# Performance work log

Measured on AMD Instinct MI355X. Metric: run time of the kernel, lower is better.

## Reference

```python
import jax, jax.numpy as jnp
import numpy as np

T = 2048          # num tokens (single long prefill sequence)
HID = 2048        # hidden_size
NH = 16           # num query heads
NKV = 2           # num kv heads
HD = 128          # head_dim (kv_channels)
ROPE_BASE = 10000.0


def setup_inputs() -> dict:
    key = jax.random.key(0)
    k1, k2, k3, k4, k5 = jax.random.split(key, 5)
    s = 0.02
    return {
        "hidden_states": jax.random.normal(k1, (T, HID), dtype=jnp.float32),
        "positions": jnp.arange(T, dtype=jnp.int64 if jax.config.jax_enable_x64 else jnp.int32),
        "Wq": jax.random.normal(k2, (NH * HD, HID), dtype=jnp.float32) * s,
        "Wk": jax.random.normal(k3, (NKV * HD, HID), dtype=jnp.float32) * s,
        "Wv": jax.random.normal(k4, (NKV * HD, HID), dtype=jnp.float32) * s,
        "Wo": jax.random.normal(k5, (HID, NH * HD), dtype=jnp.float32) * s,
    }


def _rope_cos_sin(positions):
    # fp32 RoPE tables, HF-style (concat of freqs with itself)
    inv_freq = 1.0 / (ROPE_BASE ** (jnp.arange(0, HD, 2, dtype=jnp.float32) / HD))
    freqs = positions.astype(jnp.float32)[:, None] * inv_freq[None, :]   # [T, HD/2]
    emb = jnp.concatenate([freqs, freqs], axis=-1)                        # [T, HD]
    return jnp.cos(emb)[:, None, :], jnp.sin(emb)[:, None, :]             # [T,1,HD]


def _rotate_half(x):
    x1, x2 = jnp.split(x, 2, axis=-1)
    return jnp.concatenate([-x2, x1], axis=-1)


def reference(hidden_states, positions, Wq, Wk, Wv, Wo):
    dtype = hidden_states.dtype
    # fused QKV projection (weights concatenated once, single GEMM)
    W_fused = jnp.concatenate([Wq, Wk, Wv], axis=0)            # [q+2kv, HID]
    qkv = hidden_states @ W_fused.T                             # [T, q+2kv]
    q, k, v = jnp.split(qkv, [NH * HD, NH * HD + NKV * HD], axis=-1)

    # fp32 RoPE on q/k
    cos, sin = _rope_cos_sin(positions)                         # [T,1,HD]
    qf = q.reshape(T, NH, HD).astype(jnp.float32)
    kf = k.reshape(T, NKV, HD).astype(jnp.float32)
    qf = qf * cos + _rotate_half(qf) * sin
    kf = kf * cos + _rotate_half(kf) * sin
    q = qf.astype(dtype)                                        # [T,NH,HD]
    k = kf.astype(dtype)                                        # [T,NKV,HD]
    v = v.reshape(T, NKV, HD)

    # causal GQA attention (same math as the paged-attention kernel on one seq)
    group = NH // NKV
    k_rep = jnp.repeat(k, group, axis=1)                        # [T,NH,HD]
    v_rep = jnp.repeat(v, group, axis=1)                        # [T,NH,HD]
    scale = HD ** -0.5
    scores = jnp.einsum('qhd,khd->hqk', q, k_rep) * scale       # [NH,T,T]
    causal = jnp.tril(jnp.ones((T, T), dtype=bool))
    scores = jnp.where(causal[None], scores, jnp.finfo(scores.dtype).min)
    probs = jax.nn.softmax(scores, axis=-1)
    attn = jnp.einsum('hqk,khd->qhd', probs, v_rep).reshape(T, NH * HD)

    return attn @ Wo.T                                          # [T, HID]
```

## Files before the change

### kernel.cpp

```cpp
#include <hip/hip_runtime.h>

#define T_TOK 2048
#define HID   2048
#define NH    16
#define NKV   2
#define HD    128
#define QDIM  (NH * HD)
#define KVDIM (NKV * HD)
#define QKVDIM (QDIM + 2 * KVDIM)

typedef float          f32x4  __attribute__((ext_vector_type(4)));
typedef unsigned short u16x8  __attribute__((ext_vector_type(8)));
typedef __bf16         bf16x8 __attribute__((ext_vector_type(8)));

__device__ __forceinline__ unsigned short f2bf(float f) {
    __bf16 h = (__bf16)f;
    return __builtin_bit_cast(unsigned short, h);
}
__device__ __forceinline__ float bf2f(unsigned short u) {
    return (float)__builtin_bit_cast(__bf16, u);
}

__device__ __forceinline__ f32x4 mfma16(u16x8 a, u16x8 b, f32x4 c) {
    return __builtin_amdgcn_mfma_f32_16x16x32_bf16(
        __builtin_bit_cast(bf16x8, a), __builtin_bit_cast(bf16x8, b), c, 0, 0, 0);
}

#define QSCL 0.12751743f
#define DEFER_THR 11.5416f

__global__ __launch_bounds__(256) void pack_bf16_all(
    const float* __restrict__ hidden, const float* __restrict__ Wq,
    const float* __restrict__ Wk, const float* __restrict__ Wv,
    const float* __restrict__ Wo,
    unsigned short* __restrict__ hb, unsigned short* __restrict__ Wf,
    unsigned short* __restrict__ Wob)
{
    const int b = blockIdx.x;
    const float* src; unsigned short* dst; size_t off;
    if      (b < 2048) { src = hidden; dst = hb;            off = (size_t)b * 2048; }
    else if (b < 4096) { src = Wq;     dst = Wf;            off = (size_t)(b - 2048) * 2048; }
    else if (b < 4352) { src = Wk;     dst = Wf + 4194304;  off = (size_t)(b - 4096) * 2048; }
    else if (b < 4608) { src = Wv;     dst = Wf + 4718592;  off = (size_t)(b - 4352) * 2048; }
    else               { src = Wo;     dst = Wob;           off = (size_t)(b - 4608) * 2048; }

    const size_t i = off + threadIdx.x * 8;
    float4 f0 = *reinterpret_cast<const float4*>(src + i);
    float4 f1 = *reinterpret_cast<const float4*>(src + i + 4);
    u16x8 o;
    o[0]=f2bf(f0.x); o[1]=f2bf(f0.y); o[2]=f2bf(f0.z); o[3]=f2bf(f0.w);
    o[4]=f2bf(f1.x); o[5]=f2bf(f1.y); o[6]=f2bf(f1.z); o[7]=f2bf(f1.w);
    *reinterpret_cast<u16x8*>(dst + i) = o;
}

template<bool BF16OUT>
__global__ __launch_bounds__(256) void gemm_bf16(
    const unsigned short* __restrict__ A,
    const unsigned short* __restrict__ B,
    void* __restrict__ Cv,
    int K, int NC, int nbx)
{
    __shared__ alignas(16) unsigned short As[2][128 * 64];
    __shared__ alignas(16) unsigned short Bs[2][128 * 64];

    const int tid  = threadIdx.x;
    const int lane = tid & 63;
    const int w    = tid >> 6;
    const int lg   = lane >> 4, lc = lane & 15;

    const int cpx = gridDim.x >> 3;
    const int wg  = (blockIdx.x & 7) * cpx + (blockIdx.x >> 3);
    const int m0  = (wg / nbx) * 128, n0 = (wg % nbx) * 128;

    const int rowL = lane >> 3;
    const int gS   = (lane & 7) ^ rowL;
    const int wr   = (w >> 1) * 64, wc = (w & 1) * 64;

    f32x4 acc[4][4] = {};

    auto stage = [&](int buf, int kb) {
        #pragma unroll
        for (int ci = 0; ci < 4; ci++) {
            const int chunk = w * 4 + ci;
            const int row   = chunk * 8 + rowL;
            const unsigned short* gpA = &A[(size_t)(m0 + row) * K + kb + gS * 8];
            __builtin_amdgcn_global_load_lds(
                (const __attribute__((address_space(1))) void*)gpA,
                (__attribute__((address_space(3))) void*)(&As[buf][chunk * 512]),
                16, 0, 0);
            const unsigned short* gpB = &B[(size_t)(n0 + row) * K + kb + gS * 8];
            __builtin_amdgcn_global_load_lds(
                (const __attribute__((address_space(1))) void*)gpB,
                (__attribute__((address_space(3))) void*)(&Bs[buf][chunk * 512]),
                16, 0, 0);
        }
    };

    stage(0, 0);
    const int nk = K >> 6;
    for (int t = 0; t < nk; ++t) {
        if (t + 1 < nk) {
            stage((t + 1) & 1, (t + 1) * 64);
            asm volatile("s_waitcnt vmcnt(8)" ::: "memory");
        } else {
            asm volatile("s_waitcnt vmcnt(0)" ::: "memory");
        }
        __syncthreads();

        const unsigned short* As_ = As[t & 1];
        const unsigned short* Bs_ = Bs[t & 1];
        #pragma unroll
        for (int kk = 0; kk < 2; kk++) {
            u16x8 af[4], bf[4];
            #pragma unroll
            for (int mi = 0; mi < 4; mi++) {
                const int r = wr + mi * 16 + lc;
                const int g = (kk * 4 + lg) ^ (lc & 7);
                af[mi] = *reinterpret_cast<const u16x8*>(&As_[r * 64 + g * 8]);
            }
            #pragma unroll
            for (int ni = 0; ni < 4; ni++) {
                const int r = wc + ni * 16 + lc;
                const int g = (kk * 4 + lg) ^ (lc & 7);
                bf[ni] = *reinterpret_cast<const u16x8*>(&Bs_[r * 64 + g * 8]);
            }
            #pragma unroll
            for (int mi = 0; mi < 4; mi++)
                #pragma unroll
                for (int ni = 0; ni < 4; ni++)
                    acc[mi][ni] = mfma16(af[mi], bf[ni], acc[mi][ni]);
        }
        __syncthreads();
    }

    #pragma unroll
    for (int mi = 0; mi < 4; mi++)
        #pragma unroll
        for (int ni = 0; ni < 4; ni++)
            #pragma unroll
            for (int j = 0; j < 4; j++) {
                const size_t idx = (size_t)(m0 + wr + mi * 16 + lg * 4 + j) * NC
                                   + n0 + wc + ni * 16 + lc;
                if constexpr (BF16OUT)
                    ((unsigned short*)Cv)[idx] = f2bf(acc[mi][ni][j]);
                else
                    ((float*)Cv)[idx] = acc[mi][ni][j];
            }
}

__global__ __launch_bounds__(256) void rope_kernel(
    const unsigned short* __restrict__ qkvb,
    const int* __restrict__ positions,
    unsigned short* __restrict__ qr,
    unsigned short* __restrict__ kr)
{
    const int t   = blockIdx.x;
    const int tid = threadIdx.x;
    __shared__ float cosv[64], sinv[64];

    if (tid < 64) {
        float invf = expf(-(float)tid * 0.14391156831212787f);
        float f = (float)positions[t] * invf;
        cosv[tid] = cosf(f);
        sinv[tid] = sinf(f);
    }
    __syncthreads();

    const unsigned short* row = qkvb + (size_t)t * QKVDIM;

    for (int i = tid; i < NH * 64; i += 256) {
        int hh = i >> 6, j = i & 63;
        float x1 = bf2f(row[hh * HD + j]);
        float x2 = bf2f(row[hh * HD + j + 64]);
        float c = cosv[j], s = sinv[j];
        qr[(size_t)t * QDIM + hh * HD + j]      = f2bf((x1 * c - x2 * s) * QSCL);
        qr[(size_t)t * QDIM + hh * HD + j + 64] = f2bf((x2 * c + x1 * s) * QSCL);
    }
    if (tid < NKV * 64) {
        int hh = tid >> 6, j = tid & 63;
        float x1 = bf2f(row[QDIM + hh * HD + j]);
        float x2 = bf2f(row[QDIM + hh * HD + j + 64]);
        float c = cosv[j], s = sinv[j];
        kr[(size_t)t * KVDIM + hh * HD + j]      = f2bf(x1 * c - x2 * s);
        kr[(size_t)t * KVDIM + hh * HD + j + 64] = f2bf(x2 * c + x1 * s);
    }
}

__global__ __launch_bounds__(256) void v_transpose(
    const unsigned short* __restrict__ qkvb,
    unsigned short* __restrict__ vt)
{
    __shared__ unsigned short tile[64][72];
    const int tid = threadIdx.x;
    const int t0  = blockIdx.x * 64;
    const int d0  = blockIdx.y * 64;

    {
        int r = tid >> 2;
        int c = (tid & 3) * 16;
        const unsigned short* src =
            &qkvb[(size_t)(t0 + r) * QKVDIM + QDIM + KVDIM + d0 + c];
        *reinterpret_cast<u16x8*>(&tile[r][c])     = *reinterpret_cast<const u16x8*>(src);
        *reinterpret_cast<u16x8*>(&tile[r][c + 8]) = *reinterpret_cast<const u16x8*>(src + 8);
    }
    __syncthreads();
    {
        int dr = tid >> 3;
        int tc = (tid & 7) * 8;
        #pragma unroll
        for (int i = 0; i < 2; i++) {
            int d = dr + i * 32;
            u16x8 ov;
            #pragma unroll
            for (int e = 0; e < 8; e++) ov[e] = tile[tc + e][d];
            *reinterpret_cast<u16x8*>(&vt[(size_t)(d0 + d) * T_TOK + t0 + tc]) = ov;
        }
    }
}

__global__ __launch_bounds__(256) void attn_kernel(
    const unsigned short* __restrict__ q,
    const unsigned short* __restrict__ k,
    const unsigned short* __restrict__ vt,
    unsigned short* __restrict__ o,
    float* __restrict__ pO,
    float* __restrict__ pML)
{
    __shared__ alignas(16) unsigned short Ks[2][64 * 128];
    __shared__ alignas(16) unsigned short Vs[2][128 * 64];
    __shared__ alignas(16) unsigned short P[4][16][72];

    const int tid  = threadIdx.x;
    const int lane = tid & 63;
    const int w    = tid >> 6;
    const int lg   = lane >> 4, lc = lane & 15;
    const int b    = blockIdx.x;
    const int h    = b & 15;
    const int idx  = b >> 4;

    int tau, c0;
    if (idx <= 16)      { tau = 15 + idx; c0 = 0; }
    else if (idx == 17) { tau = 31;       c0 = 1; }
    else {
        int j = idx - 18, kk = 15 - (j >> 1);
        if ((j & 1) == 0) { tau = kk - 1;  c0 = 0; }
        else              { tau = kk + 15; c0 = 1; }
    }
    const int kstart = c0 << 4;
    const int kcnt   = min(16, tau + 1 - kstart);

    const int q0   = tau * 64 + w * 16;
    const int hk   = h >> 3;
    const int xr   = (lc & 7) << 4;

    const int krow_l = (lane >> 4);
    const int kgS    = (lane & 15);
    const int vrow_l = (lane >> 3);
    const int vgS    = (lane & 7);

    u16x8 qf[4];
    #pragma unroll
    for (int dc = 0; dc < 4; dc++)
        qf[dc] = *reinterpret_cast<const u16x8*>(
            &q[(size_t)(q0 + lc) * QDIM + h * HD + dc * 32 + lg * 8]);

    float mrow = -1e30f, ell = 0.f;
    f32x4 oacc[8] = {};

    auto stage = [&](int buf, int kb) {
        #pragma unroll
        for (int ci = 0; ci < 4; ci++) {
            const int chunk = w * 4 + ci;
            const int row   = chunk * 4 + krow_l;
            const int gSk   = kgS ^ (row & 7);
            const unsigned short* gp =
                &k[(size_t)(kb + row) * KVDIM + hk * HD + gSk * 8];
            __builtin_amdgcn_global_load_lds(
                (const __attribute__((address_space(1))) void*)gp,
                (__attribute__((address_space(3))) void*)(&Ks[buf][chunk * 512]),
                16, 0, 0);
        }
        #pragma unroll
        for (int ci = 0; ci < 4; ci++) {
            const int chunk = w * 4 + ci;
            const int dr    = chunk * 8 + vrow_l;
            const int gSv   = vgS ^ (dr & 7);
            const unsigned short* gp =
                &vt[(size_t)(hk * HD + dr) * T_TOK + kb + gSv * 8];
            __builtin_amdgcn_global_load_lds(
                (const __attribute__((address_space(1))) void*)gp,
                (__attribute__((address_space(3))) void*)(&Vs[buf][chunk * 512]),
                16, 0, 0);
        }
    };

    stage(0, kstart * 64);
    for (int it = 0; it < kcnt; ++it) {
        if (it + 1 < kcnt) {
            stage((it + 1) & 1, (kstart + it + 1) * 64);
            asm volatile("s_waitcnt vmcnt(8)" ::: "memory");
        } else {
            asm volatile("s_waitcnt vmcnt(0)" ::: "memory");
        }
        __syncthreads();

        const int kb = (kstart + it) * 64;
        const char* KsB = (const char*)Ks[it & 1];
        const char* VsB = (const char*)Vs[it & 1];

        float sc[4][4];
        const bool dia = (kb + 63 > q0);
        #pragma unroll
        for (int c4 = 0; c4 < 4; c4++) {
            const int row = c4 * 16 + lc;
            f32x4 s = {0.f, 0.f, 0.f, 0.f};
            #pragma unroll
            for (int dc = 0; dc < 4; dc++) {
                u16x8 kf = *reinterpret_cast<const u16x8*>(
                    KsB + row * 256 + ((dc * 64 + lg * 16) ^ xr));
                s = mfma16(kf, qf[dc], s);
            }
            if (dia) {
                #pragma unroll
                for (int j = 0; j < 4; j++) {
                    const int kpos = kb + c4 * 16 + lg * 4 + j;
                    sc[c4][j] = (kpos <= q0 + lc) ? s[j] : -1e30f;
                }
            } else {
                #pragma unroll
                for (int j = 0; j < 4; j++) sc[c4][j] = s[j];
            }
        }

        float t01 = fmaxf(fmaxf(sc[0][0], sc[0][1]), fmaxf(sc[0][2], sc[0][3]));
        float t23 = fmaxf(fmaxf(sc[1][0], sc[1][1]), fmaxf(sc[1][2], sc[1][3]));
        float t45 = fmaxf(fmaxf(sc[2][0], sc[2][1]), fmaxf(sc[2][2], sc[2][3]));
        float t67 = fmaxf(fmaxf(sc[3][0], sc[3][1]), fmaxf(sc[3][2], sc[3][3]));
        float tmx = fmaxf(fmaxf(t01, t23), fmaxf(t45, t67));
        tmx = fmaxf(tmx, __shfl_xor(tmx, 16));
        tmx = fmaxf(tmx, __shfl_xor(tmx, 32));

        float mn;
        if (__all(tmx <= mrow + DEFER_THR)) {
            mn = mrow;
        } else {
            mn = fmaxf(mrow, tmx);
            float alpha = __builtin_amdgcn_exp2f(mrow - mn);
            mrow = mn;
            ell *= alpha;
            float aj[4];
            #pragma unroll
            for (int j = 0; j < 4; j++)
                aj[j] = __shfl(alpha, lg * 4 + j);
            #pragma unroll
            for (int d8 = 0; d8 < 8; d8++)
                #pragma unroll
                for (int j = 0; j < 4; j++)
                    oacc[d8][j] *= aj[j];
        }

        float rs = 0.f;
        #pragma unroll
        for (int c4 = 0; c4 < 4; c4++) {
            float p0 = __builtin_amdgcn_exp2f(sc[c4][0] - mn);
            float p1 = __builtin_amdgcn_exp2f(sc[c4][1] - mn);
            float p2 = __builtin_amdgcn_exp2f(sc[c4][2] - mn);
            float p3 = __builtin_amdgcn_exp2f(sc[c4][3] - mn);
            rs += (p0 + p1) + (p2 + p3);
            ushort4 pk;
            pk.x = f2bf(p0); pk.y = f2bf(p1); pk.z = f2bf(p2); pk.w = f2bf(p3);
            *reinterpret_cast<ushort4*>(&P[w][lc][c4 * 16 + lg * 4]) = pk;
        }
        rs += __shfl_xor(rs, 16);
        rs += __shfl_xor(rs, 32);
        ell += rs;

        asm volatile("s_waitcnt lgkmcnt(0)" ::: "memory");
        __builtin_amdgcn_sched_barrier(0);

        u16x8 pf0 = *reinterpret_cast<const u16x8*>(&P[w][lc][lg * 8]);
        u16x8 pf1 = *reinterpret_cast<const u16x8*>(&P[w][lc][32 + lg * 8]);

        #pragma unroll
        for (int d8 = 0; d8 < 8; d8++) {
            const int drow = d8 * 16 + lc;
            u16x8 vf0 = *reinterpret_cast<const u16x8*>(
                VsB + drow * 128 + ((lg * 16) ^ xr));
            u16x8 vf1 = *reinterpret_cast<const u16x8*>(
                VsB + drow * 128 + ((lg * 16 + 64) ^ xr));
            oacc[d8] = mfma16(pf0, vf0, oacc[d8]);
            oacc[d8] = mfma16(pf1, vf1, oacc[d8]);
        }
        __syncthreads();
    }

    if (tau < 16) {
        float ej[4];
        #pragma unroll
        for (int j = 0; j < 4; j++)
            ej[j] = __shfl(ell, lg * 4 + j);
        #pragma unroll
        for (int d8 = 0; d8 < 8; d8++)
            #pragma unroll
            for (int j = 0; j < 4; j++) {
                float val = oacc[d8][j] / ej[j];
                o[(size_t)(q0 + lg * 4 + j) * QDIM + h * HD + d8 * 16 + lc] = f2bf(val);
            }
    } else {
        const int s = (h * 16 + (tau - 16)) * 2 + c0;
        float* po = pO + (size_t)s * 8192;
        #pragma unroll
        for (int d8 = 0; d8 < 8; d8++)
            #pragma unroll
            for (int j = 0; j < 4; j++)
                po[(w * 16 + lg * 4 + j) * 128 + d8 * 16 + lc] = oacc[d8][j];
        if (lg == 0) {
            pML[s * 128 + w * 16 + lc]      = mrow;
            pML[s * 128 + 64 + w * 16 + lc] = ell;
        }
    }
}

__global__ __launch_bounds__(256) void attn_combine(
    const float* __restrict__ pO,
    const float* __restrict__ pML,
    unsigned short* __restrict__ o)
{
    const int b  = blockIdx.x;
    const int h  = b >> 4, ti = b & 15;
    const int tau = 16 + ti;
    const int s0 = (h * 16 + ti) * 2, s1 = s0 + 1;

    const int tid = threadIdx.x;
    const int r   = tid >> 2;
    const int cg  = (tid & 3) * 32;

    const float m1 = pML[s0 * 128 + r],      m2 = pML[s1 * 128 + r];
    const float l1 = pML[s0 * 128 + 64 + r], l2 = pML[s1 * 128 + 64 + r];
    const float M  = fmaxf(m1, m2);
    const float w1 = __builtin_amdgcn_exp2f(m1 - M);
    const float w2 = __builtin_amdgcn_exp2f(m2 - M);
    const float rn = 1.0f / (w1 * l1 + w2 * l2);

    const float* o1 = pO + (size_t)s0 * 8192 + r * 128 + cg;
    const float* o2 = pO + (size_t)s1 * 8192 + r * 128 + cg;
    unsigned short* dst = o + (size_t)(tau * 64 + r) * QDIM + h * HD + cg;

    #pragma unroll
    for (int i = 0; i < 8; i++) {
        float4 a = *reinterpret_cast<const float4*>(o1 + i * 4);
        float4 c = *reinterpret_cast<const float4*>(o2 + i * 4);
        ushort4 pk;
        pk.x = f2bf((w1 * a.x + w2 * c.x) * rn);
        pk.y = f2bf((w1 * a.y + w2 * c.y) * rn);
        pk.z = f2bf((w1 * a.z + w2 * c.z) * rn);
        pk.w = f2bf((w1 * a.w + w2 * c.w) * rn);
        *reinterpret_cast<ushort4*>(dst + i * 4) = pk;
    }
}

extern "C" void kernel_launch(void* const* d_in, const int* in_sizes, int n_in,
                              void* d_out, int out_size, void* d_ws, size_t ws_size,
                              hipStream_t stream) {
    const float* hidden    = (const float*)d_in[0];
    const int*   positions = (const int*)d_in[1];
    const float* Wq        = (const float*)d_in[2];
    const float* Wk        = (const float*)d_in[3];
    const float* Wv        = (const float*)d_in[4];
    const float* Wo        = (const float*)d_in[5];
    float*       out       = (float*)d_out;

    char* ws = (char*)d_ws;
    unsigned short* qkvb = (unsigned short*)(ws);
    unsigned short* qr  = (unsigned short*)(ws + 20971520);
    unsigned short* kr  = (unsigned short*)(ws + 29360128);
    unsigned short* vt  = (unsigned short*)(ws + 30408704);
    unsigned short* att = (unsigned short*)(ws + 31457280);
    unsigned short* hb  = (unsigned short*)(ws + 39845888);
    unsigned short* Wf  = (unsigned short*)(ws + 48234496);
    unsigned short* Wob = (unsigned short*)(ws + 58720256);
    float* pO  = (float*)(ws);
    float* pML = (float*)(ws + 16777216);

    pack_bf16_all<<<6656, 256, 0, stream>>>(hidden, Wq, Wk, Wv, Wo, hb, Wf, Wob);
    gemm_bf16<true><<<320, 256, 0, stream>>>(hb, Wf, qkvb, HID, QKVDIM, QKVDIM / 128);
    rope_kernel<<<T_TOK, 256, 0, stream>>>(qkvb, positions, qr, kr);
    v_transpose<<<dim3(T_TOK / 64, KVDIM / 64), 256, 0, stream>>>(qkvb, vt);
    attn_kernel<<<NH * 48, 256, 0, stream>>>(qr, kr, vt, att, pO, pML);
    attn_combine<<<256, 256, 0, stream>>>(pO, pML, att);
    gemm_bf16<false><<<256, 256, 0, stream>>>(att, Wob, out, QDIM, HID, HID / 128);
}
```

Measured before the change: 145.6 us.

## Halve GEMM M-tile, merge rope and V-transpose, single-buffer attention LDS

The GEMM tile drops from 128x128 to 64x128, which doubles the grid to 640 and 512 workgroups and halves per-thread accumulators and A-tile LDS. The rope and V-transpose kernels are merged into one launch dispatched by block index. The attention kernel drops K/V double buffering for a single buffer, loading each tile inside the loop with extra barriers; this cuts LDS use but exposes load latency. Together these trade more blocks and occupancy against less latency hiding and more B-tile reloads.

New measurement: 130.3 us. 10.5% less time.

```diff
diff --git a/kernel.cpp b/kernel.cpp
--- a/kernel.cpp
+++ b/kernel.cpp
@@ -60,7 +60,7 @@
     void* __restrict__ Cv,
     int K, int NC, int nbx)
 {
-    __shared__ alignas(16) unsigned short As[2][128 * 64];
+    __shared__ alignas(16) unsigned short As[2][64 * 64];
     __shared__ alignas(16) unsigned short Bs[2][128 * 64];
 
     const int tid  = threadIdx.x;
@@ -70,24 +70,29 @@
 
     const int cpx = gridDim.x >> 3;
     const int wg  = (blockIdx.x & 7) * cpx + (blockIdx.x >> 3);
-    const int m0  = (wg / nbx) * 128, n0 = (wg % nbx) * 128;
+    const int m0  = (wg / nbx) * 64, n0 = (wg % nbx) * 128;
 
     const int rowL = lane >> 3;
     const int gS   = (lane & 7) ^ rowL;
-    const int wr   = (w >> 1) * 64, wc = (w & 1) * 64;
-
-    f32x4 acc[4][4] = {};
+    const int wr   = (w >> 1) * 32, wc = (w & 1) * 64;
+
+    f32x4 acc[2][4] = {};
 
     auto stage = [&](int buf, int kb) {
         #pragma unroll
-        for (int ci = 0; ci < 4; ci++) {
-            const int chunk = w * 4 + ci;
+        for (int ci = 0; ci < 2; ci++) {
+            const int chunk = w * 2 + ci;
             const int row   = chunk * 8 + rowL;
             const unsigned short* gpA = &A[(size_t)(m0 + row) * K + kb + gS * 8];
             __builtin_amdgcn_global_load_lds(
                 (const __attribute__((address_space(1))) void*)gpA,
                 (__attribute__((address_space(3))) void*)(&As[buf][chunk * 512]),
                 16, 0, 0);
+        }
+        #pragma unroll
+        for (int ci = 0; ci < 4; ci++) {
+            const int chunk = w * 4 + ci;
+            const int row   = chunk * 8 + rowL;
             const unsigned short* gpB = &B[(size_t)(n0 + row) * K + kb + gS * 8];
             __builtin_amdgcn_global_load_lds(
                 (const __attribute__((address_space(1))) void*)gpB,
@@ -101,7 +106,7 @@
     for (int t = 0; t < nk; ++t) {
         if (t + 1 < nk) {
             stage((t + 1) & 1, (t + 1) * 64);
-            asm volatile("s_waitcnt vmcnt(8)" ::: "memory");
+            asm volatile("s_waitcnt vmcnt(6)" ::: "memory");
         } else {
             asm volatile("s_waitcnt vmcnt(0)" ::: "memory");
         }
@@ -111,21 +116,20 @@
         const unsigned short* Bs_ = Bs[t & 1];
         #pragma unroll
         for (int kk = 0; kk < 2; kk++) {
-            u16x8 af[4], bf[4];
-            #pragma unroll
-            for (int mi = 0; mi < 4; mi++) {
+            u16x8 af[2], bf[4];
+            const int g = (kk * 4 + lg) ^ (lc & 7);
+            #pragma unroll
+            for (int mi = 0; mi < 2; mi++) {
                 const int r = wr + mi * 16 + lc;
-                const int g = (kk * 4 + lg) ^ (lc & 7);
                 af[mi] = *reinterpret_cast<const u16x8*>(&As_[r * 64 + g * 8]);
             }
             #pragma unroll
             for (int ni = 0; ni < 4; ni++) {
                 const int r = wc + ni * 16 + lc;
-                const int g = (kk * 4 + lg) ^ (lc & 7);
                 bf[ni] = *reinterpret_cast<const u16x8*>(&Bs_[r * 64 + g * 8]);
             }
             #pragma unroll
-            for (int mi = 0; mi < 4; mi++)
+            for (int mi = 0; mi < 2; mi++)
                 #pragma unroll
                 for (int ni = 0; ni < 4; ni++)
                     acc[mi][ni] = mfma16(af[mi], bf[ni], acc[mi][ni]);
@@ -134,7 +138,7 @@
     }
 
     #pragma unroll
-    for (int mi = 0; mi < 4; mi++)
+    for (int mi = 0; mi < 2; mi++)
         #pragma unroll
         for (int ni = 0; ni < 4; ni++)
             #pragma unroll
@@ -148,72 +152,68 @@
             }
 }
 
-__global__ __launch_bounds__(256) void rope_kernel(
+__global__ __launch_bounds__(256) void rope_vt(
     const unsigned short* __restrict__ qkvb,
     const int* __restrict__ positions,
     unsigned short* __restrict__ qr,
-    unsigned short* __restrict__ kr)
-{
-    const int t   = blockIdx.x;
-    const int tid = threadIdx.x;
-    __shared__ float cosv[64], sinv[64];
-
-    if (tid < 64) {
-        float invf = expf(-(float)tid * 0.14391156831212787f);
-        float f = (float)positions[t] * invf;
-        cosv[tid] = cosf(f);
-        sinv[tid] = sinf(f);
-    }
-    __syncthreads();
-
-    const unsigned short* row = qkvb + (size_t)t * QKVDIM;
-
-    for (int i = tid; i < NH * 64; i += 256) {
-        int hh = i >> 6, j = i & 63;
-        float x1 = bf2f(row[hh * HD + j]);
-        float x2 = bf2f(row[hh * HD + j + 64]);
-        float c = cosv[j], s = sinv[j];
-        qr[(size_t)t * QDIM + hh * HD + j]      = f2bf((x1 * c - x2 * s) * QSCL);
-        qr[(size_t)t * QDIM + hh * HD + j + 64] = f2bf((x2 * c + x1 * s) * QSCL);
-    }
-    if (tid < NKV * 64) {
-        int hh = tid >> 6, j = tid & 63;
-        float x1 = bf2f(row[QDIM + hh * HD + j]);
-        float x2 = bf2f(row[QDIM + hh * HD + j + 64]);
-        float c = cosv[j], s = sinv[j];
-        kr[(size_t)t * KVDIM + hh * HD + j]      = f2bf(x1 * c - x2 * s);
-        kr[(size_t)t * KVDIM + hh * HD + j + 64] = f2bf(x2 * c + x1 * s);
-    }
-}
-
-__global__ __launch_bounds__(256) void v_transpose(
-    const unsigned short* __restrict__ qkvb,
+    unsigned short* __restrict__ kr,
     unsigned short* __restrict__ vt)
 {
+    __shared__ float cosv[64], sinv[64];
     __shared__ unsigned short tile[64][72];
     const int tid = threadIdx.x;
-    const int t0  = blockIdx.x * 64;
-    const int d0  = blockIdx.y * 64;
-
-    {
-        int r = tid >> 2;
-        int c = (tid & 3) * 16;
-        const unsigned short* src =
-            &qkvb[(size_t)(t0 + r) * QKVDIM + QDIM + KVDIM + d0 + c];
-        *reinterpret_cast<u16x8*>(&tile[r][c])     = *reinterpret_cast<const u16x8*>(src);
-        *reinterpret_cast<u16x8*>(&tile[r][c + 8]) = *reinterpret_cast<const u16x8*>(src + 8);
-    }
-    __syncthreads();
-    {
-        int dr = tid >> 3;
-        int tc = (tid & 7) * 8;
-        #pragma unroll
-        for (int i = 0; i < 2; i++) {
-            int d = dr + i * 32;
-            u16x8 ov;
-            #pragma unroll
-            for (int e = 0; e < 8; e++) ov[e] = tile[tc + e][d];
-            *reinterpret_cast<u16x8*>(&vt[(size_t)(d0 + d) * T_TOK + t0 + tc]) = ov;
+
+    if (blockIdx.x < 2048) {
+        const int t = blockIdx.x;
+        if (tid < 64) {
+            float invf = expf(-(float)tid * 0.14391156831212787f);
+            float f = (float)positions[t] * invf;
+            cosv[tid] = cosf(f);
+            sinv[tid] = sinf(f);
+        }
+        __syncthreads();
+
+        const unsigned short* row = qkvb + (size_t)t * QKVDIM;
+        for (int i = tid; i < NH * 64; i += 256) {
+            int hh = i >> 6, j = i & 63;
+            float x1 = bf2f(row[hh * HD + j]);
+            float x2 = bf2f(row[hh * HD + j + 64]);
+            float c = cosv[j], s = sinv[j];
+            qr[(size_t)t * QDIM + hh * HD + j]      = f2bf((x1 * c - x2 * s) * QSCL);
+            qr[(size_t)t * QDIM + hh * HD + j + 64] = f2bf((x2 * c + x1 * s) * QSCL);
+        }
+        if (tid < NKV * 64) {
+            int hh = tid >> 6, j = tid & 63;
+            float x1 = bf2f(row[QDIM + hh * HD + j]);
+            float x2 = bf2f(row[QDIM + hh * HD + j + 64]);
+            float c = cosv[j], s = sinv[j];
+            kr[(size_t)t * KVDIM + hh * HD + j]      = f2bf(x1 * c - x2 * s);
+            kr[(size_t)t * KVDIM + hh * HD + j + 64] = f2bf(x2 * c + x1 * s);
+        }
+    } else {
+        const int bb = blockIdx.x - 2048;
+        const int t0 = (bb & 31) * 64;
+        const int d0 = (bb >> 5) * 64;
+        {
+            int r = tid >> 2;
+            int c = (tid & 3) * 16;
+            const unsigned short* src =
+                &qkvb[(size_t)(t0 + r) * QKVDIM + QDIM + KVDIM + d0 + c];
+            *reinterpret_cast<u16x8*>(&tile[r][c])     = *reinterpret_cast<const u16x8*>(src);
+            *reinterpret_cast<u16x8*>(&tile[r][c + 8]) = *reinterpret_cast<const u16x8*>(src + 8);
+        }
+        __syncthreads();
+        {
+            int dr = tid >> 3;
+            int tc = (tid & 7) * 8;
+            #pragma unroll
+            for (int i = 0; i < 2; i++) {
+                int d = dr + i * 32;
+                u16x8 ov;
+                #pragma unroll
+                for (int e = 0; e < 8; e++) ov[e] = tile[tc + e][d];
+                *reinterpret_cast<u16x8*>(&vt[(size_t)(d0 + d) * T_TOK + t0 + tc]) = ov;
+            }
         }
     }
 }
@@ -226,8 +226,8 @@
     float* __restrict__ pO,
     float* __restrict__ pML)
 {
-    __shared__ alignas(16) unsigned short Ks[2][64 * 128];
-    __shared__ alignas(16) unsigned short Vs[2][128 * 64];
+    __shared__ alignas(16) unsigned short Ks[64 * 128];
+    __shared__ alignas(16) unsigned short Vs[128 * 64];
     __shared__ alignas(16) unsigned short P[4][16][72];
 
     const int tid  = threadIdx.x;
@@ -267,7 +267,7 @@
     float mrow = -1e30f, ell = 0.f;
     f32x4 oacc[8] = {};
 
-    auto stage = [&](int buf, int kb) {
+    auto stage = [&](int kb) {
         #pragma unroll
         for (int ci = 0; ci < 4; ci++) {
             const int chunk = w * 4 + ci;
@@ -277,7 +277,7 @@
                 &k[(size_t)(kb + row) * KVDIM + hk * HD + gSk * 8];
             __builtin_amdgcn_global_load_lds(
                 (const __attribute__((address_space(1))) void*)gp,
-                (__attribute__((address_space(3))) void*)(&Ks[buf][chunk * 512]),
+                (__attribute__((address_space(3))) void*)(&Ks[chunk * 512]),
                 16, 0, 0);
         }
         #pragma unroll
@@ -289,24 +289,19 @@
                 &vt[(size_t)(hk * HD + dr) * T_TOK + kb + gSv * 8];
             __builtin_amdgcn_global_load_lds(
                 (const __attribute__((address_space(1))) void*)gp,
-                (__attribute__((address_space(3))) void*)(&Vs[buf][chunk * 512]),
+                (__attribute__((address_space(3))) void*)(&Vs[chunk * 512]),
                 16, 0, 0);
         }
     };
 
-    stage(0, kstart * 64);
     for (int it = 0; it < kcnt; ++it) {
-        if (it + 1 < kcnt) {
-            stage((it + 1) & 1, (kstart + it + 1) * 64);
-            asm volatile("s_waitcnt vmcnt(8)" ::: "memory");
-        } else {
-            asm volatile("s_waitcnt vmcnt(0)" ::: "memory");
-        }
-        __syncthreads();
-
         const int kb = (kstart + it) * 64;
-        const char* KsB = (const char*)Ks[it & 1];
-        const char* VsB = (const char*)Vs[it & 1];
+        stage(kb);
+        asm volatile("s_waitcnt vmcnt(4)" ::: "memory");
+        __syncthreads();
+
+        const char* KsB = (const char*)Ks;
+        const char* VsB = (const char*)Vs;
 
         float sc[4][4];
         const bool dia = (kb + 63 > q0);
@@ -375,8 +370,9 @@
         rs += __shfl_xor(rs, 32);
         ell += rs;
 
-        asm volatile("s_waitcnt lgkmcnt(0)" ::: "memory");
+        asm volatile("s_waitcnt vmcnt(0) lgkmcnt(0)" ::: "memory");
         __builtin_amdgcn_sched_barrier(0);
+        __syncthreads();
 
         u16x8 pf0 = *reinterpret_cast<const u16x8*>(&P[w][lc][lg * 8]);
         u16x8 pf1 = *reinterpret_cast<const u16x8*>(&P[w][lc][32 + lg * 8]);
@@ -391,7 +387,7 @@
             oacc[d8] = mfma16(pf0, vf0, oacc[d8]);
             oacc[d8] = mfma16(pf1, vf1, oacc[d8]);
         }
-        __syncthreads();
+        if (it + 1 < kcnt) __syncthreads();
     }
 
     if (tau < 16) {
@@ -483,10 +479,9 @@
     float* pML = (float*)(ws + 16777216);
 
     pack_bf16_all<<<6656, 256, 0, stream>>>(hidden, Wq, Wk, Wv, Wo, hb, Wf, Wob);
-    gemm_bf16<true><<<320, 256, 0, stream>>>(hb, Wf, qkvb, HID, QKVDIM, QKVDIM / 128);
-    rope_kernel<<<T_TOK, 256, 0, stream>>>(qkvb, positions, qr, kr);
-    v_transpose<<<dim3(T_TOK / 64, KVDIM / 64), 256, 0, stream>>>(qkvb, vt);
+    gemm_bf16<true><<<640, 256, 0, stream>>>(hb, Wf, qkvb, HID, QKVDIM, QKVDIM / 128);
+    rope_vt<<<2176, 256, 0, stream>>>(qkvb, positions, qr, kr, vt);
     attn_kernel<<<NH * 48, 256, 0, stream>>>(qr, kr, vt, att, pO, pML);
     attn_combine<<<256, 256, 0, stream>>>(pO, pML, att);
-    gemm_bf16<false><<<256, 256, 0, stream>>>(att, Wob, out, QDIM, HID, HID / 128);
-}
+    gemm_bf16<false><<<512, 256, 0, stream>>>(att, Wob, out, QDIM, HID, HID / 128);
+}
```
